# Kernel tuning notes

Hardware: AMD Instinct MI355X
Metric: run time of the kernel (lower is better)

Reference implementation:

```python
import jax, jax.numpy as jnp
import numpy as np

DIM = 1024
HIDDEN = 3072
SCALE = 1.0 / 127.0  # fixed Q8_0-style dequant scale from QuantizedLinear


def setup_inputs() -> dict:
    key = jax.random.key(0)
    k_x, k_g, k_u, k_d = jax.random.split(key, 4)
    x = jax.random.normal(k_x, (4, 2048, DIM), dtype=jnp.float32)
    # int8-valued quantized weights stored as int32 (symmetric range like torch int8 weights)
    w_gate = jax.random.randint(k_g, (HIDDEN, DIM), -127, 128, dtype=jnp.int32)
    w_up = jax.random.randint(k_u, (HIDDEN, DIM), -127, 128, dtype=jnp.int32)
    w_down = jax.random.randint(k_d, (DIM, HIDDEN), -127, 128, dtype=jnp.int32)
    return {"x": x, "w_gate": w_gate, "w_up": w_up, "w_down": w_down}


def _dequant(w_int, dtype):
    return w_int.astype(dtype) * jnp.asarray(SCALE, dtype)


def reference(x, w_gate, w_up, w_down):
    # QuantizedLinear: dequantize int8 weight to x.dtype, then F.linear (x @ W^T)
    wg = _dequant(w_gate, x.dtype)   # [H, D]
    wu = _dequant(w_up, x.dtype)     # [H, D]
    wd = _dequant(w_down, x.dtype)   # [D, H]
    gate = jnp.einsum('bsd,hd->bsh', x, wg)
    up = jnp.einsum('bsd,hd->bsh', x, wu)
    h = jax.nn.silu(gate) * up       # SwiGLU elementwise fusion
    return jnp.einsum('bsh,dh->bsd', h, wd)
```

## Files before the change

kernel.cpp:

```cpp
#include <hip/hip_runtime.h>
#include <hip/hip_bf16.h>


typedef __attribute__((ext_vector_type(8))) __bf16 bf16x8;
typedef __attribute__((ext_vector_type(4))) float f32x4;

static constexpr float QS = 1.0f / 127.0f;

__device__ __forceinline__ void gload_lds16(const void* g, void* l) {
  __builtin_amdgcn_global_load_lds(
      (const __attribute__((address_space(1))) void*)g,
      (__attribute__((address_space(3))) void*)l,
      16, 0, 0);
}


__global__ __launch_bounds__(256) void k_conv_x(const float* __restrict__ x,
                                                __bf16* __restrict__ xb, int n8) {
  int t = blockIdx.x * 256 + threadIdx.x;
  if (t >= n8) return;
  const float4* p = (const float4*)(x + (size_t)t * 8);
  float4 a = p[0], b = p[1];
  bf16x8 o;
  o[0] = (__bf16)a.x; o[1] = (__bf16)a.y; o[2] = (__bf16)a.z; o[3] = (__bf16)a.w;
  o[4] = (__bf16)b.x; o[5] = (__bf16)b.y; o[6] = (__bf16)b.z; o[7] = (__bf16)b.w;
  *(bf16x8*)(xb + (size_t)t * 8) = o;
}

__global__ __launch_bounds__(256) void k_conv_w1(const int* __restrict__ wg,
                                                 const int* __restrict__ wu,
                                                 __bf16* __restrict__ w1) {
  int t = blockIdx.x * 256 + threadIdx.x;
  int c8 = t & 127;
  int v = t >> 7;
  int bb = v >> 5, tt = v & 31;
  const int* src = (tt < 16) ? (wg + (size_t)(bb * 16 + tt) * 1024)
                             : (wu + (size_t)(bb * 16 + (tt & 15)) * 1024);
  const int4* p = (const int4*)(src + c8 * 8);
  int4 a = p[0], b = p[1];
  bf16x8 o;
  o[0] = (__bf16)(float)a.x; o[1] = (__bf16)(float)a.y;
  o[2] = (__bf16)(float)a.z; o[3] = (__bf16)(float)a.w;
  o[4] = (__bf16)(float)b.x; o[5] = (__bf16)(float)b.y;
  o[6] = (__bf16)(float)b.z; o[7] = (__bf16)(float)b.w;
  *(bf16x8*)(w1 + (size_t)v * 1024 + c8 * 8) = o;
}

__global__ __launch_bounds__(256) void k_conv_wd(const int* __restrict__ wdn,
                                                 __bf16* __restrict__ wdb, int n8) {
  int t = blockIdx.x * 256 + threadIdx.x;
  if (t >= n8) return;
  const int4* p = (const int4*)(wdn + (size_t)t * 8);
  int4 a = p[0], b = p[1];
  bf16x8 o;
  o[0] = (__bf16)(float)a.x; o[1] = (__bf16)(float)a.y;
  o[2] = (__bf16)(float)a.z; o[3] = (__bf16)(float)a.w;
  o[4] = (__bf16)(float)b.x; o[5] = (__bf16)(float)b.y;
  o[6] = (__bf16)(float)b.z; o[7] = (__bf16)(float)b.w;
  *(bf16x8*)(wdb + (size_t)t * 8) = o;
}

template <bool SWIGLU>
__global__ __launch_bounds__(256) void k_gemm_bt(const __bf16* __restrict__ A,
                                                 const __bf16* __restrict__ B,
                                                 void* __restrict__ Out,
                                                 int K, int ldo) {
  __shared__ __bf16 sA[128][64];
  __shared__ __bf16 sB[128][64];
  const int tid = threadIdx.x;
  const int lane = tid & 63;
  const int wid = tid >> 6;
  const int wm = wid >> 1, wn = wid & 1;
  const int row0 = blockIdx.y * 128, col0 = blockIdx.x * 128;
  const int r16 = lane & 15;
  const int kq = lane >> 4;

  f32x4 acc[4][4] = {};

  const int nkt = K >> 6;
  for (int kt = 0; kt < nkt; ++kt) {
    __syncthreads();
#pragma unroll
    for (int it = 0; it < 4; ++it) {
      int chunk = it * 256 + tid;
      int r = chunk >> 3, kc = chunk & 7;
      gload_lds16(A + (size_t)(row0 + r) * K + kt * 64 + kc * 8,
                  ((__bf16*)sA) + chunk * 8);
      gload_lds16(B + (size_t)(col0 + r) * K + kt * 64 + kc * 8,
                  ((__bf16*)sB) + chunk * 8);
    }
    __syncthreads();
#pragma unroll
    for (int ks = 0; ks < 2; ++ks) {
      const int k0 = ks * 32 + kq * 8;
      bf16x8 av[4], bv[4];
#pragma unroll
      for (int i = 0; i < 4; ++i)
        av[i] = *(const bf16x8*)&sA[wm * 64 + i * 16 + r16][k0];
#pragma unroll
      for (int j = 0; j < 4; ++j)
        bv[j] = *(const bf16x8*)&sB[wn * 64 + j * 16 + r16][k0];
#pragma unroll
      for (int i = 0; i < 4; ++i)
#pragma unroll
        for (int j = 0; j < 4; ++j)
          acc[i][j] = __builtin_amdgcn_mfma_f32_16x16x32_bf16(av[i], bv[j],
                                                              acc[i][j], 0, 0, 0);
    }
  }

  if constexpr (SWIGLU) {
    __bf16* hout = (__bf16*)Out;
    const int hbase = (col0 + wn * 64) >> 1;
#pragma unroll
    for (int i = 0; i < 4; ++i) {
#pragma unroll
      for (int p = 0; p < 2; ++p) {
#pragma unroll
        for (int r = 0; r < 4; ++r) {
          int row = row0 + wm * 64 + i * 16 + kq * 4 + r;
          float g = acc[i][2 * p][r] * QS;
          float u = acc[i][2 * p + 1][r] * QS;
          float hv = (g / (1.0f + __expf(-g))) * u;
          hout[(size_t)row * ldo + hbase + p * 16 + r16] = (__bf16)hv;
        }
      }
    }
  } else {
    float* out = (float*)Out;
#pragma unroll
    for (int i = 0; i < 4; ++i)
#pragma unroll
      for (int j = 0; j < 4; ++j)
#pragma unroll
        for (int r = 0; r < 4; ++r) {
          int row = row0 + wm * 64 + i * 16 + kq * 4 + r;
          int col = col0 + wn * 64 + j * 16 + r16;
          out[(size_t)row * ldo + col] = acc[i][j][r] * QS;
        }
  }
}


extern "C" void kernel_launch(void* const* d_in, const int* in_sizes, int n_in,
                              void* d_out, int out_size, void* d_ws, size_t ws_size,
                              hipStream_t stream) {
  const float* x = (const float*)d_in[0];
  const int* wg = (const int*)d_in[1];
  const int* wu = (const int*)d_in[2];
  const int* wd = (const int*)d_in[3];

  char* ws = (char*)d_ws;
  __bf16* xb  = (__bf16*)(ws);
  __bf16* w1  = (__bf16*)(ws + 16777216);
  __bf16* wdb = (__bf16*)(ws + 16777216 + 12582912);
  __bf16* h   = (__bf16*)(ws + 35651584);

  k_conv_x<<<4096, 256, 0, stream>>>(x, xb, 1048576);
  k_conv_w1<<<3072, 256, 0, stream>>>(wg, wu, w1);
  k_conv_wd<<<1536, 256, 0, stream>>>(wd, wdb, 393216);

  k_gemm_bt<true><<<dim3(48, 64), 256, 0, stream>>>(xb, w1, h, 1024, 3072);
  k_gemm_bt<false><<<dim3(8, 64), 256, 0, stream>>>(h, wdb, (float*)d_out, 3072, 1024);
}
```

Before: 334.7 us.

## Swizzle LDS tiles and split-K the down-projection GEMM with a reduce pass

XOR-swizzles the k-chunk placement in shared memory so the MFMA operand reads avoid bank conflicts. Splits the K dimension of the down-projection GEMM across two z-slices into fp32 partial buffers, then adds them in a separate reduce kernel. This gives the small 512-block grid more parallelism. The cost is extra workspace traffic and one more launch, and split-K only runs when the workspace is large enough.

```diff
diff --git a/kernel.cpp b/kernel.cpp
--- a/kernel.cpp
+++ b/kernel.cpp
@@ -60,11 +60,12 @@
   *(bf16x8*)(wdb + (size_t)t * 8) = o;
 }
 
-template <bool SWIGLU>
+template <int MODE>
 __global__ __launch_bounds__(256) void k_gemm_bt(const __bf16* __restrict__ A,
                                                  const __bf16* __restrict__ B,
                                                  void* __restrict__ Out,
-                                                 int K, int ldo) {
+                                                 int lda, int nkt, int ldo,
+                                                 size_t zstride) {
   __shared__ __bf16 sA[128][64];
   __shared__ __bf16 sB[128][64];
   const int tid = threadIdx.x;
@@ -74,32 +75,35 @@
   const int row0 = blockIdx.y * 128, col0 = blockIdx.x * 128;
   const int r16 = lane & 15;
   const int kq = lane >> 4;
+  const int kz = blockIdx.z * nkt;
 
   f32x4 acc[4][4] = {};
 
-  const int nkt = K >> 6;
-  for (int kt = 0; kt < nkt; ++kt) {
+  for (int kt = kz; kt < kz + nkt; ++kt) {
     __syncthreads();
 #pragma unroll
     for (int it = 0; it < 4; ++it) {
       int chunk = it * 256 + tid;
       int r = chunk >> 3, kc = chunk & 7;
-      gload_lds16(A + (size_t)(row0 + r) * K + kt * 64 + kc * 8,
+      int kcs = kc ^ (r & 7);
+      gload_lds16(A + (size_t)(row0 + r) * lda + kt * 64 + kcs * 8,
                   ((__bf16*)sA) + chunk * 8);
-      gload_lds16(B + (size_t)(col0 + r) * K + kt * 64 + kc * 8,
+      gload_lds16(B + (size_t)(col0 + r) * lda + kt * 64 + kcs * 8,
                   ((__bf16*)sB) + chunk * 8);
     }
     __syncthreads();
 #pragma unroll
     for (int ks = 0; ks < 2; ++ks) {
-      const int k0 = ks * 32 + kq * 8;
+      const int chs = ((ks * 4 + kq) ^ (r16 & 7)) << 4;
       bf16x8 av[4], bv[4];
 #pragma unroll
       for (int i = 0; i < 4; ++i)
-        av[i] = *(const bf16x8*)&sA[wm * 64 + i * 16 + r16][k0];
+        av[i] = *(const bf16x8*)(((const char*)sA) +
+                                 (wm * 64 + i * 16 + r16) * 128 + chs);
 #pragma unroll
       for (int j = 0; j < 4; ++j)
-        bv[j] = *(const bf16x8*)&sB[wn * 64 + j * 16 + r16][k0];
+        bv[j] = *(const bf16x8*)(((const char*)sB) +
+                                 (wn * 64 + j * 16 + r16) * 128 + chs);
 #pragma unroll
       for (int i = 0; i < 4; ++i)
 #pragma unroll
@@ -109,7 +113,7 @@
     }
   }
 
-  if constexpr (SWIGLU) {
+  if constexpr (MODE == 1) {
     __bf16* hout = (__bf16*)Out;
     const int hbase = (col0 + wn * 64) >> 1;
 #pragma unroll
@@ -127,7 +131,7 @@
       }
     }
   } else {
-    float* out = (float*)Out;
+    float* out = (float*)Out + blockIdx.z * zstride;
 #pragma unroll
     for (int i = 0; i < 4; ++i)
 #pragma unroll
@@ -139,6 +143,17 @@
           out[(size_t)row * ldo + col] = acc[i][j][r] * QS;
         }
   }
+}
+
+__global__ __launch_bounds__(256) void k_reduce2(const float* __restrict__ p,
+                                                 float* __restrict__ out, int n4) {
+  int t = blockIdx.x * 256 + threadIdx.x;
+  if (t >= n4) return;
+  const float4* a = (const float4*)p;
+  const float4* b = (const float4*)(p + (size_t)8192 * 1024);
+  float4 va = a[t], vb = b[t];
+  ((float4*)out)[t] = make_float4(va.x + vb.x, va.y + vb.y,
+                                  va.z + vb.z, va.w + vb.w);
 }
 
 
@@ -155,11 +170,21 @@
   __bf16* w1  = (__bf16*)(ws + 16777216);
   __bf16* wdb = (__bf16*)(ws + 16777216 + 12582912);
   __bf16* h   = (__bf16*)(ws + 35651584);
+  float*  part = (float*)(ws + 85983232);
+  const bool splitk = ws_size >= (size_t)85983232 + 2u * 33554432u;
 
   k_conv_x<<<4096, 256, 0, stream>>>(x, xb, 1048576);
   k_conv_w1<<<3072, 256, 0, stream>>>(wg, wu, w1);
   k_conv_wd<<<1536, 256, 0, stream>>>(wd, wdb, 393216);
 
-  k_gemm_bt<true><<<dim3(48, 64), 256, 0, stream>>>(xb, w1, h, 1024, 3072);
-  k_gemm_bt<false><<<dim3(8, 64), 256, 0, stream>>>(h, wdb, (float*)d_out, 3072, 1024);
+  k_gemm_bt<1><<<dim3(48, 64, 1), 256, 0, stream>>>(xb, w1, h, 1024, 16, 3072, 0);
+
+  if (splitk) {
+    k_gemm_bt<0><<<dim3(8, 64, 2), 256, 0, stream>>>(h, wdb, part, 3072, 24, 1024,
+                                                     (size_t)8192 * 1024);
+    k_reduce2<<<8192, 256, 0, stream>>>(part, (float*)d_out, 2097152);
+  } else {
+    k_gemm_bt<0><<<dim3(8, 64, 1), 256, 0, stream>>>(h, wdb, (float*)d_out,
+                                                     3072, 48, 1024, 0);
+  }
 }
```

After: 331.9 us. About the same (-0.8%).
